# Optimization experiments

Measured on AMD Instinct MI355X. Metric: run time of the kernel, lower is better.

Reference implementation:

```python
import jax, jax.numpy as jnp
import numpy as np

LN_EPS = 1e-5

def _ln(x, g, b):
    mu = jnp.mean(x, axis=-1, keepdims=True)
    var = jnp.mean(jnp.square(x - mu), axis=-1, keepdims=True)
    return (x - mu) * jax.lax.rsqrt(var + LN_EPS) * g + b

def _block(x, W, b, g, be):
    # Linear -> LayerNorm -> exact GELU (torch default)
    return jax.nn.gelu(_ln(x @ W + b, g, be), approximate=False)

def setup_inputs() -> dict:
    key = jax.random.key(0)
    ks = iter(jax.random.split(key, 32))
    N, D, C, K = 500000, 256, 8192, 8192
    enc_w = [3, 64, 128, 256]
    dec_w = [D, 512, 512, 512]
    d = {"points": jax.random.normal(next(ks), (N, 3), jnp.float32)}
    for i in range(3):
        fi, fo = enc_w[i], enc_w[i + 1]
        d[f"eW{i}"] = jax.random.normal(next(ks), (fi, fo), jnp.float32) / np.sqrt(fi)
        d[f"eb{i}"] = jnp.zeros((fo,), jnp.float32)
        d[f"eg{i}"] = jnp.ones((fo,), jnp.float32)
        d[f"ebeta{i}"] = jnp.zeros((fo,), jnp.float32)
    d["oW"] = jax.random.normal(next(ks), (256, D), jnp.float32) / 16.0
    d["ob"] = jnp.zeros((D,), jnp.float32)
    d["codebook"] = jax.random.normal(next(ks), (C, D), jnp.float32)
    for i in range(3):
        fi, fo = dec_w[i], dec_w[i + 1]
        d[f"dW{i}"] = jax.random.normal(next(ks), (fi, fo), jnp.float32) / np.sqrt(fi)
        d[f"db{i}"] = jnp.zeros((fo,), jnp.float32)
        d[f"dg{i}"] = jnp.ones((fo,), jnp.float32)
        d[f"dbeta{i}"] = jnp.zeros((fo,), jnp.float32)
    d["doW"] = jax.random.normal(next(ks), (512, K * 3), jnp.float32) / np.sqrt(512)
    d["dob"] = jnp.zeros((K * 3,), jnp.float32)
    return d

def reference(points, eW0, eb0, eg0, ebeta0, eW1, eb1, eg1, ebeta1, eW2, eb2, eg2, ebeta2,
              oW, ob, codebook,
              dW0, db0, dg0, dbeta0, dW1, db1, dg1, dbeta1, dW2, db2, dg2, dbeta2,
              doW, dob):
    # --- encode_continuous: per-point MLP then max-pool over N ---
    h = _block(points, eW0, eb0, eg0, ebeta0)
    h = _block(h, eW1, eb1, eg1, ebeta1)
    h = _block(h, eW2, eb2, eg2, ebeta2)  # (N, 256)
    pooled = jnp.max(h, axis=0)           # (256,)
    z_e = pooled @ oW + ob                # (D,)
    # --- quantize: squared-distance argmin over codebook, then gather ---
    dists = jnp.sum(z_e * z_e) - 2.0 * (codebook @ z_e) + jnp.sum(codebook * codebook, axis=-1)  # (C,)
    idx = jnp.argmin(dists)
    z_q = codebook[idx]                   # (D,)
    # --- straight-through ---
    z_q_st = z_e + jax.lax.stop_gradient(z_q - z_e)
    # --- decode ---
    g = _block(z_q_st, dW0, db0, dg0, dbeta0)
    g = _block(g, dW1, db1, dg1, dbeta1)
    g = _block(g, dW2, db2, dg2, dbeta2)
    recon = (g @ doW + dob).reshape(-1, 3)  # (K, 3)
    return recon, z_e, z_q
```

## Files before the change

### kernel.cpp

```cpp
#include <hip/hip_runtime.h>
#include <math.h>

#define NBLK 256

typedef float    f32x4 __attribute__((ext_vector_type(4)));
typedef _Float16 f16x4 __attribute__((ext_vector_type(4)));
typedef _Float16 f16x2 __attribute__((ext_vector_type(2)));
typedef _Float16 f16x8 __attribute__((ext_vector_type(8)));

#define MFMA16(A,B,C) __builtin_amdgcn_mfma_f32_16x16x16f16((A),(B),(C),0,0,0)

__device__ __forceinline__ float fast_rcp(float x) {
#if __has_builtin(__builtin_amdgcn_rcpf)
    return __builtin_amdgcn_rcpf(x);
#else
    return 1.0f / x;
#endif
}

__device__ __forceinline__ float gelu_exact(float x) {
    float u  = x * 0.70710678118654752440f;
    float au = fabsf(u);
    float t  = fast_rcp(fmaf(0.3275911f, au, 1.0f));
    float p  = t * fmaf(t, fmaf(t, fmaf(t, fmaf(t, 1.061405429f, -1.453152027f),
                       1.421413741f), -0.284496736f), 0.254829592f);
    float e  = __expf(-(au * au));
    float er = fmaf(-p, e, 1.0f);
    er = copysignf(er, u);
    return 0.5f * x * (1.0f + er);
}

__device__ __forceinline__ f16x2 pk_from(float a, float b) {
#if __has_builtin(__builtin_amdgcn_cvt_pkrtz)
    auto r = __builtin_amdgcn_cvt_pkrtz(a, b);
    f16x2 out;
    __builtin_memcpy(&out, &r, sizeof(out));
    return out;
#else
    return (f16x2){(_Float16)a, (_Float16)b};
#endif
}

__global__ void __launch_bounds__(512, 1)
enc_kernel(const float* __restrict__ pts, int N,
           const float* __restrict__ W0, const float* __restrict__ B0,
           const float* __restrict__ G0, const float* __restrict__ E0,
           const float* __restrict__ W1, const float* __restrict__ B1,
           const float* __restrict__ G1, const float* __restrict__ E1,
           const float* __restrict__ W2, const float* __restrict__ B2,
           const float* __restrict__ G2, const float* __restrict__ E2,
           float* __restrict__ part)
{
    __shared__ __align__(16) _Float16 w1q[8*2*64*8];
    __shared__ __align__(16) _Float16 w2q[16*4*64*8];
    __shared__ __align__(16) _Float16 actL1[8][16*132];
    __shared__ __align__(16) _Float16 scr[8][16*132];
    __shared__ __align__(16) float v1s[384];
    __shared__ __align__(16) float v2s[768];

    const int tid  = threadIdx.x;
    const int lane = tid & 63;
    const int wid  = tid >> 6;
    const int l15  = lane & 15;
    const int l4   = lane >> 4;

    #pragma unroll
    for (int e = 0; e < 2; ++e) {
        int idx = tid + e*512;
        int l = idx & 63, ks2 = (idx >> 6) & 1, nt = idx >> 7;
        f16x8 v;
        #pragma unroll
        for (int jj = 0; jj < 8; ++jj) {
            int ks = ks2*2 + (jj >> 2), j = jj & 3;
            int k  = ks*16 + ((l >> 4) << 2) + j;
            v[jj] = (_Float16)W1[k*128 + nt*16 + (l & 15)];
        }
        *(f16x8*)&w1q[idx*8] = v;
    }
    #pragma unroll
    for (int e = 0; e < 8; ++e) {
        int idx = tid + e*512;
        int l = idx & 63, ks2 = (idx >> 6) & 3, nt = idx >> 8;
        f16x8 v;
        #pragma unroll
        for (int jj = 0; jj < 8; ++jj) {
            int ks = ks2*2 + (jj >> 2), j = jj & 3;
            int k  = ks*16 + ((l >> 4) << 2) + j;
            v[jj] = (_Float16)W2[k*256 + nt*16 + (l & 15)];
        }
        *(f16x8*)&w2q[idx*8] = v;
    }
    if (tid < 128) { v1s[tid] = B1[tid]; v1s[128 + tid] = G1[tid]; v1s[256 + tid] = E1[tid]; }
    if (tid >= 256) {
        int c = tid - 256;
        v2s[c] = B2[c]; v2s[256 + c] = G2[c]; v2s[512 + c] = E2[c];
    }

    f16x4 w0f[4];
    float b0v[4], g0v[4], e0v[4];
    #pragma unroll
    for (int nt = 0; nt < 4; ++nt) {
        int ch = nt*16 + l15;
        #pragma unroll
        for (int j = 0; j < 4; ++j) {
            int k = l4*4 + j;
            w0f[nt][j] = (_Float16)((k < 3) ? W0[k*64 + ch] : 0.0f);
        }
        b0v[nt] = B0[ch]; g0v[nt] = G0[ch]; e0v[nt] = E0[ch];
    }
    __syncthreads();

    float run[16];
    #pragma unroll
    for (int nt = 0; nt < 16; ++nt) run[nt] = -INFINITY;

    const int tiles = (N + 127) >> 7;
    for (int t = blockIdx.x; t < tiles; t += NBLK) {
        const int pbase = t*128 + wid*16;
        f16x4 A0 = {(_Float16)0, (_Float16)0, (_Float16)0, (_Float16)0};
        {
            int p = pbase + l15;
            if (l4 == 0 && p < N) {
                A0[0] = (_Float16)pts[p*3];
                A0[1] = (_Float16)pts[p*3+1];
                A0[2] = (_Float16)pts[p*3+2];
            }
        }
        f32x4 acc0[4];
        #pragma unroll
        for (int nt = 0; nt < 4; ++nt) {
            acc0[nt] = (f32x4){b0v[nt], b0v[nt], b0v[nt], b0v[nt]};
            acc0[nt] = MFMA16(A0, w0f[nt], acc0[nt]);
        }
        {
            f32x4 s4 = (acc0[0] + acc0[1]) + (acc0[2] + acc0[3]);
            f32x4 q4 = (acc0[0]*acc0[0] + acc0[1]*acc0[1]) + (acc0[2]*acc0[2] + acc0[3]*acc0[3]);
            #pragma unroll
            for (int m = 1; m < 16; m <<= 1)
                #pragma unroll
                for (int i = 0; i < 4; ++i) {
                    s4[i] += __shfl_xor(s4[i], m, 64);
                    q4[i] += __shfl_xor(q4[i], m, 64);
                }
            f32x4 mu, rs;
            #pragma unroll
            for (int i = 0; i < 4; ++i) {
                float m_ = s4[i] * (1.0f/64.0f);
                float v_ = q4[i] * (1.0f/64.0f) - m_*m_;
                mu[i] = m_; rs[i] = rsqrtf(v_ + 1e-5f);
            }
            #pragma unroll
            for (int nt = 0; nt < 4; ++nt)
                #pragma unroll
                for (int r = 0; r < 4; ++r) {
                    float v = fmaf((acc0[nt][r]-mu[r])*rs[r], g0v[nt], e0v[nt]);
                    scr[wid][(l4*4+r)*68 + nt*16 + l15] = (_Float16)gelu_exact(v);
                }
        }

        f32x4 acc1[8];
        #pragma unroll
        for (int nt = 0; nt < 8; ++nt) {
            float b = v1s[nt*16 + l15];
            acc1[nt] = (f32x4){b, b, b, b};
        }
        #pragma unroll
        for (int ks2 = 0; ks2 < 2; ++ks2) {
            f16x4 Aa = *(const f16x4*)&scr[wid][l15*68 + (ks2*2+0)*16 + l4*4];
            f16x4 Ab = *(const f16x4*)&scr[wid][l15*68 + (ks2*2+1)*16 + l4*4];
            #pragma unroll
            for (int nt = 0; nt < 8; ++nt) {
                f16x8 bb = *(const f16x8*)&w1q[((nt*2 + ks2)*64 + lane)*8];
                f16x4 blo = __builtin_shufflevector(bb, bb, 0,1,2,3);
                f16x4 bhi = __builtin_shufflevector(bb, bb, 4,5,6,7);
                acc1[nt] = MFMA16(Aa, blo, acc1[nt]);
                acc1[nt] = MFMA16(Ab, bhi, acc1[nt]);
            }
        }
        {
            f32x4 s4 = ((acc1[0]+acc1[1])+(acc1[2]+acc1[3])) + ((acc1[4]+acc1[5])+(acc1[6]+acc1[7]));
            f32x4 q4 = ((acc1[0]*acc1[0]+acc1[1]*acc1[1])+(acc1[2]*acc1[2]+acc1[3]*acc1[3]))
                     + ((acc1[4]*acc1[4]+acc1[5]*acc1[5])+(acc1[6]*acc1[6]+acc1[7]*acc1[7]));
            #pragma unroll
            for (int m = 1; m < 16; m <<= 1)
                #pragma unroll
                for (int i = 0; i < 4; ++i) {
                    s4[i] += __shfl_xor(s4[i], m, 64);
                    q4[i] += __shfl_xor(q4[i], m, 64);
                }
            f32x4 mu, rs;
            #pragma unroll
            for (int i = 0; i < 4; ++i) {
                float m_ = s4[i] * (1.0f/128.0f);
                float v_ = q4[i] * (1.0f/128.0f) - m_*m_;
                mu[i] = m_; rs[i] = rsqrtf(v_ + 1e-5f);
            }
            #pragma unroll
            for (int nt = 0; nt < 8; ++nt) {
                float g = v1s[128 + nt*16 + l15], e = v1s[256 + nt*16 + l15];
                #pragma unroll
                for (int r = 0; r < 4; ++r) {
                    float v = fmaf((acc1[nt][r]-mu[r])*rs[r], g, e);
                    actL1[wid][(l4*4+r)*132 + nt*16 + l15] = (_Float16)gelu_exact(v);
                }
            }
        }

        f32x4 sT = {0,0,0,0}, qT = {0,0,0,0};
        f32x4 acc2[8];
        #pragma unroll
        for (int nt = 0; nt < 8; ++nt) {
            float b = v2s[nt*16 + l15];
            acc2[nt] = (f32x4){b, b, b, b};
        }
        #pragma unroll
        for (int ks2 = 0; ks2 < 4; ++ks2) {
            f16x4 Aa = *(const f16x4*)&actL1[wid][l15*132 + (ks2*2+0)*16 + l4*4];
            f16x4 Ab = *(const f16x4*)&actL1[wid][l15*132 + (ks2*2+1)*16 + l4*4];
            #pragma unroll
            for (int nt = 0; nt < 8; ++nt) {
                f16x8 bb = *(const f16x8*)&w2q[((nt*4 + ks2)*64 + lane)*8];
                f16x4 blo = __builtin_shufflevector(bb, bb, 0,1,2,3);
                f16x4 bhi = __builtin_shufflevector(bb, bb, 4,5,6,7);
                acc2[nt] = MFMA16(Aa, blo, acc2[nt]);
                acc2[nt] = MFMA16(Ab, bhi, acc2[nt]);
            }
        }
        #pragma unroll
        for (int nt = 0; nt < 8; ++nt) {
            sT += acc2[nt];
            qT += acc2[nt]*acc2[nt];
            f16x2 lo = pk_from(acc2[nt][0], acc2[nt][1]);
            f16x2 hi = pk_from(acc2[nt][2], acc2[nt][3]);
            f16x4 pk = (f16x4){lo[0], lo[1], hi[0], hi[1]};
            *(f16x4*)&scr[wid][(nt*64 + lane)*4] = pk;
        }
        #pragma unroll
        for (int nt = 0; nt < 8; ++nt) {
            float b = v2s[(nt+8)*16 + l15];
            acc2[nt] = (f32x4){b, b, b, b};
        }
        #pragma unroll
        for (int ks2 = 0; ks2 < 4; ++ks2) {
            f16x4 Aa = *(const f16x4*)&actL1[wid][l15*132 + (ks2*2+0)*16 + l4*4];
            f16x4 Ab = *(const f16x4*)&actL1[wid][l15*132 + (ks2*2+1)*16 + l4*4];
            #pragma unroll
            for (int nt = 0; nt < 8; ++nt) {
                f16x8 bb = *(const f16x8*)&w2q[(((nt+8)*4 + ks2)*64 + lane)*8];
                f16x4 blo = __builtin_shufflevector(bb, bb, 0,1,2,3);
                f16x4 bhi = __builtin_shufflevector(bb, bb, 4,5,6,7);
                acc2[nt] = MFMA16(Aa, blo, acc2[nt]);
                acc2[nt] = MFMA16(Ab, bhi, acc2[nt]);
            }
        }
        #pragma unroll
        for (int nt = 0; nt < 8; ++nt) {
            sT += acc2[nt];
            qT += acc2[nt]*acc2[nt];
        }
        {
            #pragma unroll
            for (int m = 1; m < 16; m <<= 1)
                #pragma unroll
                for (int i = 0; i < 4; ++i) {
                    sT[i] += __shfl_xor(sT[i], m, 64);
                    qT[i] += __shfl_xor(qT[i], m, 64);
                }
            f32x4 mu, rs;
            bool pv[4];
            #pragma unroll
            for (int i = 0; i < 4; ++i) {
                float m_ = sT[i] * (1.0f/256.0f);
                float v_ = qT[i] * (1.0f/256.0f) - m_*m_;
                mu[i] = m_; rs[i] = rsqrtf(v_ + 1e-5f);
                pv[i] = (pbase + l4*4 + i) < N;
            }
            #pragma unroll
            for (int nt = 0; nt < 8; ++nt) {
                int ch = (nt+8)*16 + l15;
                float g = v2s[256 + ch], e = v2s[512 + ch];
                float rm = -INFINITY;
                #pragma unroll
                for (int r = 0; r < 4; ++r) {
                    float v = fmaf((acc2[nt][r]-mu[r])*rs[r], g, e);
                    v = gelu_exact(v);
                    rm = fmaxf(rm, pv[r] ? v : -INFINITY);
                }
                run[nt+8] = fmaxf(run[nt+8], rm);
            }
            #pragma unroll
            for (int nt = 0; nt < 8; ++nt) {
                int ch = nt*16 + l15;
                float g = v2s[256 + ch], e = v2s[512 + ch];
                f16x4 pk = *(const f16x4*)&scr[wid][(nt*64 + lane)*4];
                float rm = -INFINITY;
                #pragma unroll
                for (int r = 0; r < 4; ++r) {
                    float raw = (float)pk[r];
                    float v = fmaf((raw-mu[r])*rs[r], g, e);
                    v = gelu_exact(v);
                    rm = fmaxf(rm, pv[r] ? v : -INFINITY);
                }
                run[nt] = fmaxf(run[nt], rm);
            }
        }
    }

    __syncthreads();
    float* pm = (float*)actL1;
    #pragma unroll
    for (int nt = 0; nt < 16; ++nt) {
        float v = run[nt];
        v = fmaxf(v, __shfl_xor(v, 16, 64));
        v = fmaxf(v, __shfl_xor(v, 32, 64));
        if (l4 == 0) pm[wid*256 + nt*16 + l15] = v;
    }
    __syncthreads();
    if (tid < 256) {
        float v = pm[tid];
        #pragma unroll
        for (int w = 1; w < 8; ++w) v = fmaxf(v, pm[w*256 + tid]);
        part[(size_t)blockIdx.x * 256 + tid] = v;
    }
}

__global__ void __launch_bounds__(256)
pool_ze_kernel(const float* __restrict__ part, const float* __restrict__ oW,
               const float* __restrict__ ob, float* __restrict__ out_ze,
               float* __restrict__ ws_ze)
{
    __shared__ float pooled[256];
    const int j = threadIdx.x;
    float m0 = -INFINITY, m1 = -INFINITY, m2 = -INFINITY, m3 = -INFINITY;
    for (int b = 0; b < NBLK; b += 4) {
        m0 = fmaxf(m0, part[(b+0)*256 + j]);
        m1 = fmaxf(m1, part[(b+1)*256 + j]);
        m2 = fmaxf(m2, part[(b+2)*256 + j]);
        m3 = fmaxf(m3, part[(b+3)*256 + j]);
    }
    pooled[j] = fmaxf(fmaxf(m0, m1), fmaxf(m2, m3));
    __syncthreads();
    float a0 = 0.f, a1 = 0.f;
    for (int k = 0; k < 256; k += 2) {
        a0 = fmaf(pooled[k],   oW[(k  )*256 + j], a0);
        a1 = fmaf(pooled[k+1], oW[(k+1)*256 + j], a1);
    }
    float z = (a0 + a1) + ob[j];
    out_ze[j] = z;
    ws_ze[j]  = z;
}

__global__ void __launch_bounds__(256)
quant_kernel(const float* __restrict__ cb, const float* __restrict__ ze,
             float* __restrict__ qpart)
{
    const int lane = threadIdx.x & 63;
    const int wid  = threadIdx.x >> 6;
    const int gw   = (int)blockIdx.x * 4 + wid;
    const float4* cb4 = (const float4*)cb;
    const float4* z4p = (const float4*)ze;
    const float4  z   = z4p[lane];

    float bv = INFINITY;
    int   bi = 0x7fffffff;
    for (int code = gw; code < 8192; code += 256) {
        float4 c = cb4[code*64 + lane];
        float d = c.x*c.x + c.y*c.y + c.z*c.z + c.w*c.w
                - 2.0f*(c.x*z.x + c.y*z.y + c.z*z.z + c.w*z.w);
        #pragma unroll
        for (int m = 1; m < 64; m <<= 1) d += __shfl_xor(d, m, 64);
        if (d < bv) { bv = d; bi = code; }
    }
    __shared__ float sv[4];
    __shared__ int   si[4];
    if (lane == 0) { sv[wid] = bv; si[wid] = bi; }
    __syncthreads();
    if (threadIdx.x == 0) {
        float v = sv[0]; int i = si[0];
        for (int w = 1; w < 4; ++w)
            if (sv[w] < v || (sv[w] == v && si[w] < i)) { v = sv[w]; i = si[w]; }
        qpart[blockIdx.x*2]     = v;
        qpart[blockIdx.x*2 + 1] = __int_as_float(i);
    }
}

template<int KIN>
__device__ __forceinline__ void dec_block_body(const float* xs, const float* __restrict__ W,
        const float* __restrict__ B, const float* __restrict__ G,
        const float* __restrict__ E, float* __restrict__ xout, float* red)
{
    const int j = threadIdx.x;
    float a0=0,a1=0,a2=0,a3=0;
    for (int k = 0; k < KIN; k += 4) {
        a0 = fmaf(xs[k  ], W[(k  )*512 + j], a0);
        a1 = fmaf(xs[k+1], W[(k+1)*512 + j], a1);
        a2 = fmaf(xs[k+2], W[(k+2)*512 + j], a2);
        a3 = fmaf(xs[k+3], W[(k+3)*512 + j], a3);
    }
    float acc = ((a0+a1)+(a2+a3)) + B[j];
    float s = acc, q = acc*acc;
    #pragma unroll
    for (int m = 1; m < 64; m <<= 1) { s += __shfl_xor(s, m, 64); q += __shfl_xor(q, m, 64); }
    const int wid = j >> 6, lane = j & 63;
    if (lane == 0) { red[wid*2] = s; red[wid*2+1] = q; }
    __syncthreads();
    float ts = 0.f, tq = 0.f;
    #pragma unroll
    for (int w = 0; w < 8; ++w) { ts += red[w*2]; tq += red[w*2+1]; }
    float mu  = ts * (1.0f/512.0f);
    float var = tq * (1.0f/512.0f) - mu*mu;
    float v = fmaf((acc - mu) * rsqrtf(var + 1e-5f), G[j], E[j]);
    xout[j] = gelu_exact(v);
}

__global__ void __launch_bounds__(512)
tail_kernel(const float* __restrict__ qpart, const float* __restrict__ cb,
            const float* __restrict__ ze,
            const float* __restrict__ W0d, const float* __restrict__ B0d,
            const float* __restrict__ G0d, const float* __restrict__ E0d,
            const float* __restrict__ W1d, const float* __restrict__ B1d,
            const float* __restrict__ G1d, const float* __restrict__ E1d,
            const float* __restrict__ W2d, const float* __restrict__ B2d,
            const float* __restrict__ G2d, const float* __restrict__ E2d,
            float* __restrict__ out_zq, float* __restrict__ g2_out)
{
    __shared__ float xa[512];
    __shared__ float xb[512];
    __shared__ float red[16];
    __shared__ int   sidx;
    const int j = threadIdx.x;

    if (j == 0) {
        float bv = INFINITY; int bi = 0x7fffffff;
        for (int b = 0; b < 64; ++b) {
            float v = qpart[b*2];
            int   i = __float_as_int(qpart[b*2 + 1]);
            if (v < bv || (v == bv && i < bi)) { bv = v; bi = i; }
        }
        sidx = bi;
    }
    __syncthreads();
    const int idx = sidx;

    if (j < 256) {
        float zq = cb[(size_t)idx*256 + j];
        out_zq[j] = zq;
        float z = ze[j];
        xa[j] = z + (zq - z);
    }
    __syncthreads();
    dec_block_body<256>(xa, W0d, B0d, G0d, E0d, xb, red);
    __syncthreads();

    dec_block_body<512>(xb, W1d, B1d, G1d, E1d, xa, red);
    __syncthreads();

    dec_block_body<512>(xa, W2d, B2d, G2d, E2d, xb, red);
    __syncthreads();
    g2_out[j] = xb[j];
}

__global__ void __launch_bounds__(256)
final_kernel(const float* __restrict__ g, const float* __restrict__ W,
             const float* __restrict__ B, float* __restrict__ out)
{
    __shared__ float gs[512];
    const int t = threadIdx.x;
    gs[t]       = g[t];
    gs[t + 256] = g[t + 256];
    __syncthreads();
    const int j = (int)blockIdx.x * 256 + t;
    float a0=0,a1=0,a2=0,a3=0;
    #pragma unroll 4
    for (int k = 0; k < 512; k += 4) {
        a0 = fmaf(gs[k  ], W[(size_t)(k  )*24576 + j], a0);
        a1 = fmaf(gs[k+1], W[(size_t)(k+1)*24576 + j], a1);
        a2 = fmaf(gs[k+2], W[(size_t)(k+2)*24576 + j], a2);
        a3 = fmaf(gs[k+3], W[(size_t)(k+3)*24576 + j], a3);
    }
    out[j] = ((a0+a1)+(a2+a3)) + B[j];
}

extern "C" void kernel_launch(void* const* d_in, const int* in_sizes, int n_in,
                              void* d_out, int out_size, void* d_ws, size_t ws_size,
                              hipStream_t stream)
{
    (void)n_in; (void)out_size; (void)ws_size;
    const float* pts = (const float*)d_in[0];
    const float* eW0 = (const float*)d_in[1];
    const float* eb0 = (const float*)d_in[2];
    const float* eg0 = (const float*)d_in[3];
    const float* ee0 = (const float*)d_in[4];
    const float* eW1 = (const float*)d_in[5];
    const float* eb1 = (const float*)d_in[6];
    const float* eg1 = (const float*)d_in[7];
    const float* ee1 = (const float*)d_in[8];
    const float* eW2 = (const float*)d_in[9];
    const float* eb2 = (const float*)d_in[10];
    const float* eg2 = (const float*)d_in[11];
    const float* ee2 = (const float*)d_in[12];
    const float* oW  = (const float*)d_in[13];
    const float* ob  = (const float*)d_in[14];
    const float* cb  = (const float*)d_in[15];
    const float* dW0 = (const float*)d_in[16];
    const float* db0 = (const float*)d_in[17];
    const float* dg0 = (const float*)d_in[18];
    const float* de0 = (const float*)d_in[19];
    const float* dW1 = (const float*)d_in[20];
    const float* db1 = (const float*)d_in[21];
    const float* dg1 = (const float*)d_in[22];
    const float* de1 = (const float*)d_in[23];
    const float* dW2 = (const float*)d_in[24];
    const float* db2 = (const float*)d_in[25];
    const float* dg2 = (const float*)d_in[26];
    const float* de2 = (const float*)d_in[27];
    const float* doW = (const float*)d_in[28];
    const float* dob = (const float*)d_in[29];

    float* out = (float*)d_out;
    float* ws  = (float*)d_ws;
    const int N = in_sizes[0] / 3;

    float* part = ws;
    float* ze   = ws + 262144;
    float* qp   = ws + 262400;
    float* g2   = ws + 263552;

    enc_kernel<<<NBLK, 512, 0, stream>>>(pts, N,
        eW0, eb0, eg0, ee0, eW1, eb1, eg1, ee1, eW2, eb2, eg2, ee2, part);
    pool_ze_kernel<<<1, 256, 0, stream>>>(part, oW, ob, out + 24576, ze);
    quant_kernel<<<64, 256, 0, stream>>>(cb, ze, qp);
    tail_kernel<<<1, 512, 0, stream>>>(qp, cb, ze,
        dW0, db0, dg0, de0, dW1, db1, dg1, de1, dW2, db2, dg2, de2,
        out + 24832, g2);
    final_kernel<<<96, 256, 0, stream>>>(g2, doW, dob, out);
}
```

Baseline: 329.6 us.

## Track per-channel min/max of pre-GELU values and apply GELU after pooling

GELU is decreasing below its single minimum and increasing above it, so its maximum over a set of inputs lies at either the smallest or the largest input. The encoder's last layer now keeps a running packed fp16 min/max of the LayerNorm output per channel, instead of evaluating exact GELU on every point and channel. GELU is applied only twice per channel in the final reduction, removing the per-element erf/exp cost from the hot loop. The trade-off is that the running extrema are stored in fp16 with round-toward-zero packing, which loses some precision in the pooled values.

```diff
diff --git a/kernel.cpp b/kernel.cpp
--- a/kernel.cpp
+++ b/kernel.cpp
@@ -41,6 +41,13 @@
 #endif
 }
 
+__device__ __forceinline__ f16x2 mm_update(f16x2 acc, f16x2 cand) {
+    f16x2 r;
+    r[0] = (cand[0] < acc[0]) ? cand[0] : acc[0];
+    r[1] = (cand[1] > acc[1]) ? cand[1] : acc[1];
+    return r;
+}
+
 __global__ void __launch_bounds__(512, 1)
 enc_kernel(const float* __restrict__ pts, int N,
            const float* __restrict__ W0, const float* __restrict__ B0,
@@ -110,9 +117,10 @@
     }
     __syncthreads();
 
-    float run[16];
-    #pragma unroll
-    for (int nt = 0; nt < 16; ++nt) run[nt] = -INFINITY;
+    f16x2 run[16];
+    #pragma unroll
+    for (int nt = 0; nt < 16; ++nt)
+        run[nt] = (f16x2){(_Float16)INFINITY, (_Float16)(-INFINITY)};
 
     const int tiles = (N + 127) >> 7;
     for (int t = blockIdx.x; t < tiles; t += NBLK) {
@@ -275,33 +283,31 @@
                 mu[i] = m_; rs[i] = rsqrtf(v_ + 1e-5f);
                 pv[i] = (pbase + l4*4 + i) < N;
             }
+            const bool tfull = (pbase + 16) <= N;
             #pragma unroll
             for (int nt = 0; nt < 8; ++nt) {
                 int ch = (nt+8)*16 + l15;
                 float g = v2s[256 + ch], e = v2s[512 + ch];
-                float rm = -INFINITY;
                 #pragma unroll
                 for (int r = 0; r < 4; ++r) {
                     float v = fmaf((acc2[nt][r]-mu[r])*rs[r], g, e);
-                    v = gelu_exact(v);
-                    rm = fmaxf(rm, pv[r] ? v : -INFINITY);
-                }
-                run[nt+8] = fmaxf(run[nt+8], rm);
+                    f16x2 cand = tfull ? pk_from(v, v)
+                                       : pk_from(pv[r] ? v : INFINITY, pv[r] ? v : -INFINITY);
+                    run[nt+8] = mm_update(run[nt+8], cand);
+                }
             }
             #pragma unroll
             for (int nt = 0; nt < 8; ++nt) {
                 int ch = nt*16 + l15;
                 float g = v2s[256 + ch], e = v2s[512 + ch];
                 f16x4 pk = *(const f16x4*)&scr[wid][(nt*64 + lane)*4];
-                float rm = -INFINITY;
                 #pragma unroll
                 for (int r = 0; r < 4; ++r) {
-                    float raw = (float)pk[r];
-                    float v = fmaf((raw-mu[r])*rs[r], g, e);
-                    v = gelu_exact(v);
-                    rm = fmaxf(rm, pv[r] ? v : -INFINITY);
-                }
-                run[nt] = fmaxf(run[nt], rm);
+                    float v = fmaf(((float)pk[r]-mu[r])*rs[r], g, e);
+                    f16x2 cand = tfull ? pk_from(v, v)
+                                       : pk_from(pv[r] ? v : INFINITY, pv[r] ? v : -INFINITY);
+                    run[nt] = mm_update(run[nt], cand);
+                }
             }
         }
     }
@@ -310,10 +316,14 @@
     float* pm = (float*)actL1;
     #pragma unroll
     for (int nt = 0; nt < 16; ++nt) {
-        float v = run[nt];
-        v = fmaxf(v, __shfl_xor(v, 16, 64));
-        v = fmaxf(v, __shfl_xor(v, 32, 64));
-        if (l4 == 0) pm[wid*256 + nt*16 + l15] = v;
+        float mn = (float)run[nt][0];
+        float mx = (float)run[nt][1];
+        mn = fminf(mn, __shfl_xor(mn, 16, 64)); mn = fminf(mn, __shfl_xor(mn, 32, 64));
+        mx = fmaxf(mx, __shfl_xor(mx, 16, 64)); mx = fmaxf(mx, __shfl_xor(mx, 32, 64));
+        if (l4 == 0) {
+            float v = fmaxf(gelu_exact(mn), gelu_exact(mx));
+            pm[wid*256 + nt*16 + l15] = v;
+        }
     }
     __syncthreads();
     if (tid < 256) {
```

After: 293.8 us. 10.8% less time.
